# Kernel optimization log

Measured on AMD Instinct MI355X. Metric: run time of the kernel, lower is better.

## Reference

```python
import jax, jax.numpy as jnp
import numpy as np

B, N, F_IN, F_OUT = 8, 2048, 128, 128
ALPHA = 0.1  # leaky-relu negative slope
NEG = -9e15


def setup_inputs() -> dict:
    key = jax.random.key(0)
    k1, k2, k3, k4, k5, k6 = jax.random.split(key, 6)
    s = 1.0 / np.sqrt(F_OUT)
    return {
        "x1": jax.random.normal(k1, (B, N, F_IN), dtype=jnp.float32),
        "x2": jax.random.normal(k2, (B, N, F_IN), dtype=jnp.float32),
        "cross_weight": jax.random.uniform(k3, (F_IN, F_OUT), minval=-s, maxval=s, dtype=jnp.float32),
        "friend_weight": jax.random.uniform(k4, (F_IN, F_OUT), minval=-s, maxval=s, dtype=jnp.float32),
        "self_weight": jax.random.uniform(k5, (F_IN, F_OUT), minval=-s, maxval=s, dtype=jnp.float32),
        "att_weight": jax.random.uniform(k6, (2 * F_OUT, 1), minval=-1.0, maxval=1.0, dtype=jnp.float32),
    }


def _one_set(xq, x_others, cross_weight, friend_weight, self_weight, att_weight):
    # GAT-style additive attention for one set against cross-set + friend supports.
    fo = cross_weight.shape[1]
    a_q, a_k = att_weight[:fo], att_weight[fo:]  # split additive-attention vector
    cross = jnp.concatenate([xo @ cross_weight for xo in x_others], axis=1)  # [B, M, F]
    friend = xq @ friend_weight                                              # [B, Nq, F]
    h = jnp.concatenate([cross, friend], axis=1)                             # [B, Nk, F]
    s_q = (friend @ a_q)[..., 0]  # [B, Nq]
    s_k = (h @ a_k)[..., 0]       # [B, Nk]
    e = jax.nn.leaky_relu(s_q[:, :, None] + s_k[:, None, :], negative_slope=ALPHA)  # [B, Nq, Nk]
    nq, m = xq.shape[1], cross.shape[1]
    # mask: all cross-set keys allowed; friend keys masked on the diagonal (no self-edge)
    mask = jnp.concatenate([jnp.ones((nq, m), dtype=e.dtype),
                            1.0 - jnp.eye(nq, dtype=e.dtype)], axis=1)
    att = jax.nn.softmax(jnp.where(mask > 0, e, NEG), axis=-1)  # [B, Nq, Nk]
    out = jnp.einsum('bqk,bkf->bqf', att, h)                    # [B, Nq, F]
    return out + xq @ self_weight


def reference(x1, x2, cross_weight, friend_weight, self_weight, att_weight):
    out1 = _one_set(x1, [x2], cross_weight, friend_weight, self_weight, att_weight)
    out2 = _one_set(x2, [x1], cross_weight, friend_weight, self_weight, att_weight)
    return (out1, out2)
```

## Files before the change

### kernel.cpp

```cpp
#include <hip/hip_runtime.h>
#include <hip/hip_bf16.h>
#include <stdint.h>

typedef __attribute__((ext_vector_type(8))) short short8;
typedef __attribute__((ext_vector_type(16))) float f32x16;

#define NB 8
#define NN 2048
#define NF 128
#define NK 4096
#define L2E 1.4426950408889634f

#define OFF_HT   0u
#define OFF_WCT  16777216u
#define OFF_WFT  16809984u
#define OFF_WST  16842752u
#define OFF_U1   16875520u
#define OFF_U2   16876032u
#define OFF_U3   16876544u
#define OFF_SQ   16877056u
#define OFF_SK   17008128u

__device__ __forceinline__ short f2bf(float f){
  __bf16 h = (__bf16)f;
  return __builtin_bit_cast(short, h);
}
__device__ __forceinline__ short8 pack8(float4 a, float4 b){
  short8 r;
  r[0]=f2bf(a.x); r[1]=f2bf(a.y); r[2]=f2bf(a.z); r[3]=f2bf(a.w);
  r[4]=f2bf(b.x); r[5]=f2bf(b.y); r[6]=f2bf(b.z); r[7]=f2bf(b.w);
  return r;
}

typedef const __attribute__((address_space(1))) unsigned int* gas_t;
typedef __attribute__((address_space(3))) unsigned int* las_t;
__device__ __forceinline__ void gload_lds16(const void* g, void* l){
  __builtin_amdgcn_global_load_lds((gas_t)g, (las_t)l, 16, 0, 0);
}

__global__ __launch_bounds__(256) void k_prep(const float* __restrict__ Wc,
                                              const float* __restrict__ Wf,
                                              const float* __restrict__ Ws,
                                              const float* __restrict__ att,
                                              char* __restrict__ ws){
  int bidx = blockIdx.x, tid = threadIdx.x;
  if (bidx < 12){
    __shared__ float tile[32][129];
    int m = bidx >> 2, tno = bidx & 3;
    const float* W = (m == 0) ? Wc : ((m == 1) ? Wf : Ws);
    short* WT = (short*)(ws + ((m == 0) ? OFF_WCT : ((m == 1) ? OFF_WFT : OFF_WST)));
    int r0 = tno*32;
    #pragma unroll
    for (int i = 0; i < 16; i++){
      int e = tid + i*256;
      tile[e >> 7][e & 127] = W[(r0 + (e >> 7))*NF + (e & 127)];
    }
    __syncthreads();
    #pragma unroll
    for (int i = 0; i < 16; i++){
      int o = tid + i*256;
      int col = o >> 5, rr = o & 31;
      WT[col*NF + r0 + rr] = f2bf(tile[rr][col]);
    }
  } else {
    int wid = tid >> 6, lane = tid & 63;
    float aq0 = att[lane],      aq1 = att[64 + lane];
    float ak0 = att[NF + lane], ak1 = att[NF + 64 + lane];
    float* u1 = (float*)(ws + OFF_U1);
    float* u2 = (float*)(ws + OFF_U2);
    float* u3 = (float*)(ws + OFF_U3);
    for (int j = 0; j < 32; j++){
      int r = wid*32 + j;
      float wf0 = Wf[r*NF + lane], wf1 = Wf[r*NF + 64 + lane];
      float wc0 = Wc[r*NF + lane], wc1 = Wc[r*NF + 64 + lane];
      float s1 = wf0*aq0 + wf1*aq1;
      float s2 = wc0*ak0 + wc1*ak1;
      float s3 = wf0*ak0 + wf1*ak1;
      #pragma unroll
      for (int d = 1; d < 64; d <<= 1){
        s1 += __shfl_xor(s1, d); s2 += __shfl_xor(s2, d); s3 += __shfl_xor(s3, d);
      }
      if (lane == 0){ u1[r] = s1; u2[r] = s2; u3[r] = s3; }
    }
  }
}

__global__ __launch_bounds__(256) void k_build(const float* __restrict__ x1,
                                               const float* __restrict__ x2,
                                               char* __restrict__ ws){
  int bid = blockIdx.x;
  int xid  = bid >> 7;
  int b    = (bid >> 4) & 7;
  int tile = bid & 15;
  int tid = threadIdx.x, wid = tid >> 6, lane = tid & 63;
  int l31 = lane & 31, khalf = lane >> 5;
  int r0 = tile*128 + wid*32;
  int row = r0 + l31;

  const float* x = xid ? x2 : x1;
  const float* u1 = (const float*)(ws + OFF_U1);
  const float* u2 = (const float*)(ws + OFF_U2);
  const float* u3 = (const float*)(ws + OFF_U3);
  const float* xrow = x + (size_t)(b*NN + row)*NF;

  short8 aF[8];
  float p1=0.f, p2=0.f, p3=0.f;
  #pragma unroll
  for (int ks = 0; ks < 8; ks++){
    int k0 = ks*16 + khalf*8;
    float4 xa = *(const float4*)(xrow + k0);
    float4 xb = *(const float4*)(xrow + k0 + 4);
    float4 a1 = *(const float4*)(u1 + k0), b1 = *(const float4*)(u1 + k0 + 4);
    float4 a2 = *(const float4*)(u2 + k0), b2 = *(const float4*)(u2 + k0 + 4);
    float4 a3 = *(const float4*)(u3 + k0), b3 = *(const float4*)(u3 + k0 + 4);
    p1 += xa.x*a1.x + xa.y*a1.y + xa.z*a1.z + xa.w*a1.w
        + xb.x*b1.x + xb.y*b1.y + xb.z*b1.z + xb.w*b1.w;
    p2 += xa.x*a2.x + xa.y*a2.y + xa.z*a2.z + xa.w*a2.w
        + xb.x*b2.x + xb.y*b2.y + xb.z*b2.z + xb.w*b2.w;
    p3 += xa.x*a3.x + xa.y*a3.y + xa.z*a3.z + xa.w*a3.w
        + xb.x*b3.x + xb.y*b3.y + xb.z*b3.z + xb.w*b3.w;
    aF[ks] = pack8(xa, xb);
  }
  p1 += __shfl_xor(p1, 32);
  p2 += __shfl_xor(p2, 32);
  p3 += __shfl_xor(p3, 32);
  if (lane < 32){
    float* sq = (float*)(ws + OFF_SQ);
    float* sk = (float*)(ws + OFF_SK);
    sq[(xid*NB + b)*NN + row] = p1*L2E;
    sk[(xid*NB + b)*NK + NN + row] = p3*L2E;
    sk[((1 - xid)*NB + b)*NK + row] = p2*L2E;
  }

  short* hT = (short*)(ws + OFF_HT);
  #pragma unroll
  for (int g = 0; g < 2; g++){
    const short* W = g ? (const short*)(ws + OFF_WFT) : (const short*)(ws + OFF_WCT);
    int dset = g ? xid : (1 - xid);
    int kb2  = (g ? NN : 0) + r0;
    f32x16 acc[4] = {};
    #pragma unroll
    for (int ks = 0; ks < 8; ks++){
      #pragma unroll
      for (int cb = 0; cb < 4; cb++){
        short8 bF = *(const short8*)(W + (cb*32 + l31)*NF + ks*16 + khalf*8);
        acc[cb] = __builtin_amdgcn_mfma_f32_32x32x16_bf16(aF[ks], bF, acc[cb], 0, 0, 0);
      }
    }
    short* hbase = hT + (size_t)(dset*NB + b)*NF*NK;
    #pragma unroll
    for (int cb = 0; cb < 4; cb++){
      short* hc = hbase + (size_t)(cb*32 + l31)*NK;
      #pragma unroll
      for (int g4 = 0; g4 < 4; g4++){
        int kr = kb2 + g4*8 + khalf*4;
        uint2 v;
        v.x = (unsigned)(unsigned short)f2bf(acc[cb][4*g4+0]) |
              ((unsigned)(unsigned short)f2bf(acc[cb][4*g4+1]) << 16);
        v.y = (unsigned)(unsigned short)f2bf(acc[cb][4*g4+2]) |
              ((unsigned)(unsigned short)f2bf(acc[cb][4*g4+3]) << 16);
        *(uint2*)(hc + kr) = v;
      }
    }
  }
}

__global__ __launch_bounds__(512) void k_attn(const float* __restrict__ x1,
                                              const float* __restrict__ x2,
                                              const char* __restrict__ ws,
                                              float* __restrict__ out){
  __shared__ float skb[NK];
  __shared__ __align__(16) char stg[6*16384];
  __shared__ float wmax[8];

  int hw = blockIdx.x;
  int bid = (hw & 7)*32 + (hw >> 3);
  int set = bid >> 7, b = (bid >> 4) & 7, qt = bid & 15;
  int tid = threadIdx.x, wid = tid >> 6, lane = tid & 63;
  int grp = wid >> 2, rw = wid & 3;
  int l31 = lane & 31, khalf = lane >> 5;

  const short* hT  = (const short*)(ws + OFF_HT) + (size_t)(set*NB + b)*NF*NK;
  const float* skg = (const float*)(ws + OFF_SK) + (set*NB + b)*NK;
  const float* sqg = (const float*)(ws + OFF_SQ) + (set*NB + b)*NN;
  const short* WsT = (const short*)(ws + OFF_WST);

  auto stage = [&](int li, int bufi){
    char* dst = stg + (grp*3 + bufi)*16384;
    int ch = grp*32 + li;
    #pragma unroll
    for (int i = 0; i < 4; i++){
      int q = (rw*4 + i)*64 + lane;
      int col = q >> 3, k16 = q & 7;
      int srcc = k16 ^ (col & 7);
      gload_lds16((const void*)(hT + col*NK + ch*64 + srcc*8),
                  (void*)(dst + (rw*4 + i)*1024));
    }
  };

  stage(0, 0);
  stage(1, 1);
  float mx = -3.0e38f;
  #pragma unroll
  for (int i = 0; i < 2; i++){
    int idx = i*2048 + tid*4;
    float4 v = *(const float4*)(skg + idx);
    *(float4*)(skb + idx) = v;
    mx = fmaxf(mx, fmaxf(fmaxf(v.x, v.y), fmaxf(v.z, v.w)));
  }
  #pragma unroll
  for (int d = 1; d < 64; d <<= 1) mx = fmaxf(mx, __shfl_xor(mx, d));
  if (lane == 0) wmax[wid] = mx;
  asm volatile("s_waitcnt lgkmcnt(0)" ::: "memory");
  asm volatile("s_barrier" ::: "memory");

  float skmax = wmax[0];
  #pragma unroll
  for (int i = 1; i < 8; i++) skmax = fmaxf(skmax, wmax[i]);

  int q0w = qt*128 + rw*32;
  int row = q0w + l31;
  float sqv = sqg[row];
  float t0 = sqv + skmax;
  float moff = fmaxf(t0, 0.1f*t0);
  float sqm = sqv - moff;
  float c9  = -0.9f*moff;
  int kdiag = NN + row;
  int chd = (NN + q0w) >> 6;
  int ksd = (q0w & 63) >> 4;

  f32x16 acc[4] = {};
  float zacc = 0.f;

  int bs = 2, bc = 0;
  for (int it = 0; it < 32; ++it){
    if (it < 30){
      stage(it + 2, bs);
      asm volatile("s_waitcnt vmcnt(8)" ::: "memory");
    } else if (it == 30){
      asm volatile("s_waitcnt vmcnt(4)" ::: "memory");
    } else {
      asm volatile("s_waitcnt vmcnt(0)" ::: "memory");
    }
    asm volatile("s_barrier" ::: "memory");

    int ch = grp*32 + it;
    const char* buf = stg + (grp*3 + bc)*16384;
    #pragma unroll
    for (int ks = 0; ks < 4; ks++){
      const float* skp = skb + ch*64 + ks*16 + khalf*8;
      float wv[8];
      #pragma unroll
      for (int j = 0; j < 8; j++){
        float p = skp[j] + sqm;
        float qn = __builtin_fmaf(0.1f, p, c9);
        wv[j] = __builtin_amdgcn_exp2f(fmaxf(p, qn));
      }
      if (ch == chd && (ks & ~1) == ksd){
        int kg0 = ch*64 + ks*16 + khalf*8;
        #pragma unroll
        for (int j = 0; j < 8; j++) wv[j] = (kg0 + j == kdiag) ? 0.f : wv[j];
      }
      #pragma unroll
      for (int j = 0; j < 8; j++) zacc += wv[j];
      short8 aw;
      #pragma unroll
      for (int j = 0; j < 8; j++) aw[j] = f2bf(wv[j]);
      #pragma unroll
      for (int cb = 0; cb < 4; cb++){
        int col = cb*32 + l31;
        int slot = (ks*2 + khalf) ^ (col & 7);
        short8 bF = *(const short8*)(buf + col*128 + slot*16);
        acc[cb] = __builtin_amdgcn_mfma_f32_32x32x16_bf16(aw, bF, acc[cb], 0, 0, 0);
      }
    }
    asm volatile("s_barrier" ::: "memory");
    bs = (bs == 2) ? 0 : bs + 1;
    bc = (bc == 2) ? 0 : bc + 1;
  }

  float* xch = (float*)stg;
  float* zx  = skb;
  if (grp == 1){
    #pragma unroll
    for (int cb = 0; cb < 4; cb++)
      #pragma unroll
      for (int r = 0; r < 16; r++)
        xch[(cb*16 + r)*256 + rw*64 + lane] = acc[cb][r];
    zx[rw*64 + lane] = zacc;
  }
  __syncthreads();
  if (grp == 0){
    #pragma unroll
    for (int cb = 0; cb < 4; cb++)
      #pragma unroll
      for (int r = 0; r < 16; r++)
        acc[cb][r] += xch[(cb*16 + r)*256 + rw*64 + lane];
    zacc += zx[rw*64 + lane];
    zacc += __shfl_xor(zacc, 32);
    float rz = 1.0f / zacc;
    float rzv[16];
    #pragma unroll
    for (int r = 0; r < 16; r++){
      int rowc = (r & 3) + 8*(r >> 2) + 4*khalf;
      rzv[r] = __shfl(rz, rowc);
    }
    #pragma unroll
    for (int cb = 0; cb < 4; cb++)
      #pragma unroll
      for (int r = 0; r < 16; r++) acc[cb][r] *= rzv[r];

    const float* x = set ? x2 : x1;
    const float* xrow = x + (size_t)(b*NN + row)*NF;
    #pragma unroll
    for (int ks8 = 0; ks8 < 8; ks8++){
      int k0 = ks8*16 + khalf*8;
      float4 xa = *(const float4*)(xrow + k0);
      float4 xb = *(const float4*)(xrow + k0 + 4);
      short8 aF = pack8(xa, xb);
      #pragma unroll
      for (int cb = 0; cb < 4; cb++){
        short8 bF = *(const short8*)(WsT + (cb*32 + l31)*NF + k0);
        acc[cb] = __builtin_amdgcn_mfma_f32_32x32x16_bf16(aF, bF, acc[cb], 0, 0, 0);
      }
    }
    float* op = out + (size_t)(set*NB + b)*NN*NF;
    #pragma unroll
    for (int cb = 0; cb < 4; cb++){
      #pragma unroll
      for (int r = 0; r < 16; r++){
        int rowc = (r & 3) + 8*(r >> 2) + 4*khalf;
        op[(size_t)(q0w + rowc)*NF + cb*32 + l31] = acc[cb][r];
      }
    }
  }
}

extern "C" void kernel_launch(void* const* d_in, const int* in_sizes, int n_in,
                              void* d_out, int out_size, void* d_ws, size_t ws_size,
                              hipStream_t stream){
  const float* x1  = (const float*)d_in[0];
  const float* x2  = (const float*)d_in[1];
  const float* Wc  = (const float*)d_in[2];
  const float* Wf  = (const float*)d_in[3];
  const float* Ws  = (const float*)d_in[4];
  const float* att = (const float*)d_in[5];
  char* ws = (char*)d_ws;
  float* out = (float*)d_out;

  k_prep<<<dim3(13),  dim3(256), 0, stream>>>(Wc, Wf, Ws, att, ws);
  k_build<<<dim3(256), dim3(256), 0, stream>>>(x1, x2, ws);
  k_attn<<<dim3(256), dim3(512), 0, stream>>>(x1, x2, ws, out);
}
```

Baseline: 179.7 us.

## Split attention keys across four wave groups, each wave computing two row blocks

Restructures the attention kernel so each wave handles 64 query rows (two 32-row MFMA blocks) against a shared B fragment. The key range is split across four groups of two waves instead of two groups of four, and staging becomes double-buffered with larger 16KB-per-wave-pair chunks. The intent is to reuse each LDS-loaded h fragment for two MFMAs, halving LDS reads per FLOP. In exchange it doubles accumulator registers (128 floats per lane), raises LDS use to 128KB and adds a two-stage cross-group reduction with extra barriers. The launch bound of 2 blocks per CU may conflict with that LDS footprint or force register spills.

```diff
diff --git a/kernel.cpp b/kernel.cpp
--- a/kernel.cpp
+++ b/kernel.cpp
@@ -165,19 +165,19 @@
   }
 }
 
-__global__ __launch_bounds__(512) void k_attn(const float* __restrict__ x1,
+__global__ __launch_bounds__(512, 2) void k_attn(const float* __restrict__ x1,
                                               const float* __restrict__ x2,
                                               const char* __restrict__ ws,
                                               float* __restrict__ out){
   __shared__ float skb[NK];
-  __shared__ __align__(16) char stg[6*16384];
+  __shared__ __align__(16) char stg[8*16384];
   __shared__ float wmax[8];
 
   int hw = blockIdx.x;
   int bid = (hw & 7)*32 + (hw >> 3);
   int set = bid >> 7, b = (bid >> 4) & 7, qt = bid & 15;
   int tid = threadIdx.x, wid = tid >> 6, lane = tid & 63;
-  int grp = wid >> 2, rw = wid & 3;
+  int grp = wid >> 1, rw = wid & 1;
   int l31 = lane & 31, khalf = lane >> 5;
 
   const short* hT  = (const short*)(ws + OFF_HT) + (size_t)(set*NB + b)*NF*NK;
@@ -185,21 +185,20 @@
   const float* sqg = (const float*)(ws + OFF_SQ) + (set*NB + b)*NN;
   const short* WsT = (const short*)(ws + OFF_WST);
 
-  auto stage = [&](int li, int bufi){
-    char* dst = stg + (grp*3 + bufi)*16384;
-    int ch = grp*32 + li;
-    #pragma unroll
-    for (int i = 0; i < 4; i++){
-      int q = (rw*4 + i)*64 + lane;
-      int col = q >> 3, k16 = q & 7;
+  auto stage = [&](int it, int bufi){
+    char* dst = stg + (grp*2 + bufi)*16384;
+    int ch = grp*16 + it;
+    #pragma unroll
+    for (int i = 0; i < 8; i++){
+      int u = (rw*8 + i)*64 + lane;
+      int col = u >> 3, k16 = u & 7;
       int srcc = k16 ^ (col & 7);
       gload_lds16((const void*)(hT + col*NK + ch*64 + srcc*8),
-                  (void*)(dst + (rw*4 + i)*1024));
+                  (void*)(dst + (rw*8 + i)*1024));
     }
   };
 
   stage(0, 0);
-  stage(1, 1);
   float mx = -3.0e38f;
   #pragma unroll
   for (int i = 0; i < 2; i++){
@@ -218,120 +217,161 @@
   #pragma unroll
   for (int i = 1; i < 8; i++) skmax = fmaxf(skmax, wmax[i]);
 
-  int q0w = qt*128 + rw*32;
-  int row = q0w + l31;
-  float sqv = sqg[row];
-  float t0 = sqv + skmax;
-  float moff = fmaxf(t0, 0.1f*t0);
-  float sqm = sqv - moff;
-  float c9  = -0.9f*moff;
-  int kdiag = NN + row;
+  int q0w = qt*128 + rw*64;
+  float sqm[2], c9[2]; int kdiag[2];
+  #pragma unroll
+  for (int rb = 0; rb < 2; rb++){
+    int row = q0w + rb*32 + l31;
+    float sqv = sqg[row];
+    float t0 = sqv + skmax;
+    float moff = fmaxf(t0, 0.1f*t0);
+    sqm[rb] = sqv - moff;
+    c9[rb]  = -0.9f*moff;
+    kdiag[rb] = NN + row;
+  }
   int chd = (NN + q0w) >> 6;
-  int ksd = (q0w & 63) >> 4;
-
-  f32x16 acc[4] = {};
-  float zacc = 0.f;
-
-  int bs = 2, bc = 0;
-  for (int it = 0; it < 32; ++it){
-    if (it < 30){
-      stage(it + 2, bs);
+
+  f32x16 acc[2][4] = {};
+  float zacc[2] = {0.f, 0.f};
+
+  for (int it = 0; it < 16; ++it){
+    if (it < 15){
+      stage(it + 1, (it + 1) & 1);
       asm volatile("s_waitcnt vmcnt(8)" ::: "memory");
-    } else if (it == 30){
-      asm volatile("s_waitcnt vmcnt(4)" ::: "memory");
     } else {
       asm volatile("s_waitcnt vmcnt(0)" ::: "memory");
     }
     asm volatile("s_barrier" ::: "memory");
 
-    int ch = grp*32 + it;
-    const char* buf = stg + (grp*3 + bc)*16384;
+    int ch = grp*16 + it;
+    const char* buf = stg + (grp*2 + (it & 1))*16384;
     #pragma unroll
     for (int ks = 0; ks < 4; ks++){
       const float* skp = skb + ch*64 + ks*16 + khalf*8;
-      float wv[8];
-      #pragma unroll
-      for (int j = 0; j < 8; j++){
-        float p = skp[j] + sqm;
-        float qn = __builtin_fmaf(0.1f, p, c9);
-        wv[j] = __builtin_amdgcn_exp2f(fmaxf(p, qn));
-      }
-      if (ch == chd && (ks & ~1) == ksd){
-        int kg0 = ch*64 + ks*16 + khalf*8;
-        #pragma unroll
-        for (int j = 0; j < 8; j++) wv[j] = (kg0 + j == kdiag) ? 0.f : wv[j];
-      }
-      #pragma unroll
-      for (int j = 0; j < 8; j++) zacc += wv[j];
-      short8 aw;
-      #pragma unroll
-      for (int j = 0; j < 8; j++) aw[j] = f2bf(wv[j]);
+      float sv[8];
+      #pragma unroll
+      for (int j = 0; j < 8; j++) sv[j] = skp[j];
+      short8 aw[2];
+      #pragma unroll
+      for (int rb = 0; rb < 2; rb++){
+        float wv[8];
+        #pragma unroll
+        for (int j = 0; j < 8; j++){
+          float p = sv[j] + sqm[rb];
+          float qn = __builtin_fmaf(0.1f, p, c9[rb]);
+          wv[j] = __builtin_amdgcn_exp2f(fmaxf(p, qn));
+        }
+        if (ch == chd){
+          int kg0 = ch*64 + ks*16 + khalf*8;
+          #pragma unroll
+          for (int j = 0; j < 8; j++) wv[j] = (kg0 + j == kdiag[rb]) ? 0.f : wv[j];
+        }
+        #pragma unroll
+        for (int j = 0; j < 8; j++) zacc[rb] += wv[j];
+        #pragma unroll
+        for (int j = 0; j < 8; j++) aw[rb][j] = f2bf(wv[j]);
+      }
       #pragma unroll
       for (int cb = 0; cb < 4; cb++){
         int col = cb*32 + l31;
         int slot = (ks*2 + khalf) ^ (col & 7);
         short8 bF = *(const short8*)(buf + col*128 + slot*16);
-        acc[cb] = __builtin_amdgcn_mfma_f32_32x32x16_bf16(aw, bF, acc[cb], 0, 0, 0);
+        acc[0][cb] = __builtin_amdgcn_mfma_f32_32x32x16_bf16(aw[0], bF, acc[0][cb], 0, 0, 0);
+        acc[1][cb] = __builtin_amdgcn_mfma_f32_32x32x16_bf16(aw[1], bF, acc[1][cb], 0, 0, 0);
       }
     }
     asm volatile("s_barrier" ::: "memory");
-    bs = (bs == 2) ? 0 : bs + 1;
-    bc = (bc == 2) ? 0 : bc + 1;
-  }
-
-  float* xch = (float*)stg;
-  float* zx  = skb;
-  if (grp == 1){
-    #pragma unroll
-    for (int cb = 0; cb < 4; cb++)
-      #pragma unroll
-      for (int r = 0; r < 16; r++)
-        xch[(cb*16 + r)*256 + rw*64 + lane] = acc[cb][r];
-    zx[rw*64 + lane] = zacc;
+  }
+
+  float* cbuf1 = (float*)stg;
+  float* cbuf2 = (float*)(stg + 65536);
+  float* zarr  = skb;
+  if (grp == 1 || grp == 3){
+    float* dst = (grp == 1) ? cbuf1 : cbuf2;
+    #pragma unroll
+    for (int rb = 0; rb < 2; rb++){
+      #pragma unroll
+      for (int cb = 0; cb < 4; cb++)
+        #pragma unroll
+        for (int r = 0; r < 16; r++)
+          dst[(((rw*2 + rb)*4 + cb)*16 + r)*64 + lane] = acc[rb][cb][r];
+      zarr[(wid*2 + rb)*64 + lane] = zacc[rb];
+    }
+  }
+  __syncthreads();
+  if (grp == 0 || grp == 2){
+    const float* src = (grp == 0) ? cbuf1 : cbuf2;
+    int swid = (grp == 0) ? (2 + rw) : (6 + rw);
+    #pragma unroll
+    for (int rb = 0; rb < 2; rb++){
+      #pragma unroll
+      for (int cb = 0; cb < 4; cb++)
+        #pragma unroll
+        for (int r = 0; r < 16; r++)
+          acc[rb][cb][r] += src[(((rw*2 + rb)*4 + cb)*16 + r)*64 + lane];
+      zacc[rb] += zarr[(swid*2 + rb)*64 + lane];
+    }
+  }
+  __syncthreads();
+  if (grp == 2){
+    #pragma unroll
+    for (int rb = 0; rb < 2; rb++){
+      #pragma unroll
+      for (int cb = 0; cb < 4; cb++)
+        #pragma unroll
+        for (int r = 0; r < 16; r++)
+          cbuf1[(((rw*2 + rb)*4 + cb)*16 + r)*64 + lane] = acc[rb][cb][r];
+      zarr[((4 + rw)*2 + rb)*64 + lane] = zacc[rb];
+    }
   }
   __syncthreads();
   if (grp == 0){
     #pragma unroll
-    for (int cb = 0; cb < 4; cb++)
-      #pragma unroll
-      for (int r = 0; r < 16; r++)
-        acc[cb][r] += xch[(cb*16 + r)*256 + rw*64 + lane];
-    zacc += zx[rw*64 + lane];
-    zacc += __shfl_xor(zacc, 32);
-    float rz = 1.0f / zacc;
-    float rzv[16];
-    #pragma unroll
-    for (int r = 0; r < 16; r++){
-      int rowc = (r & 3) + 8*(r >> 2) + 4*khalf;
-      rzv[r] = __shfl(rz, rowc);
-    }
-    #pragma unroll
-    for (int cb = 0; cb < 4; cb++)
-      #pragma unroll
-      for (int r = 0; r < 16; r++) acc[cb][r] *= rzv[r];
-
+    for (int rb = 0; rb < 2; rb++){
+      #pragma unroll
+      for (int cb = 0; cb < 4; cb++)
+        #pragma unroll
+        for (int r = 0; r < 16; r++)
+          acc[rb][cb][r] += cbuf1[(((rw*2 + rb)*4 + cb)*16 + r)*64 + lane];
+      zacc[rb] += zarr[((4 + rw)*2 + rb)*64 + lane];
+    }
     const float* x = set ? x2 : x1;
-    const float* xrow = x + (size_t)(b*NN + row)*NF;
-    #pragma unroll
-    for (int ks8 = 0; ks8 < 8; ks8++){
-      int k0 = ks8*16 + khalf*8;
-      float4 xa = *(const float4*)(xrow + k0);
-      float4 xb = *(const float4*)(xrow + k0 + 4);
-      short8 aF = pack8(xa, xb);
-      #pragma unroll
-      for (int cb = 0; cb < 4; cb++){
-        short8 bF = *(const short8*)(WsT + (cb*32 + l31)*NF + k0);
-        acc[cb] = __builtin_amdgcn_mfma_f32_32x32x16_bf16(aF, bF, acc[cb], 0, 0, 0);
-      }
-    }
     float* op = out + (size_t)(set*NB + b)*NN*NF;
     #pragma unroll
-    for (int cb = 0; cb < 4; cb++){
+    for (int rb = 0; rb < 2; rb++){
+      float zr = zacc[rb] + __shfl_xor(zacc[rb], 32);
+      float rz = 1.0f / zr;
+      float rzv[16];
       #pragma unroll
       for (int r = 0; r < 16; r++){
         int rowc = (r & 3) + 8*(r >> 2) + 4*khalf;
-        op[(size_t)(q0w + rowc)*NF + cb*32 + l31] = acc[cb][r];
-      }
+        rzv[r] = __shfl(rz, rowc);
+      }
+      #pragma unroll
+      for (int cb = 0; cb < 4; cb++)
+        #pragma unroll
+        for (int r = 0; r < 16; r++) acc[rb][cb][r] *= rzv[r];
+
+      const float* xrow = x + (size_t)(b*NN + q0w + rb*32 + l31)*NF;
+      #pragma unroll
+      for (int ks8 = 0; ks8 < 8; ks8++){
+        int k0 = ks8*16 + khalf*8;
+        float4 xa = *(const float4*)(xrow + k0);
+        float4 xb = *(const float4*)(xrow + k0 + 4);
+        short8 aF = pack8(xa, xb);
+        #pragma unroll
+        for (int cb = 0; cb < 4; cb++){
+          short8 bF = *(const short8*)(WsT + (cb*32 + l31)*NF + k0);
+          acc[rb][cb] = __builtin_amdgcn_mfma_f32_32x32x16_bf16(aF, bF, acc[rb][cb], 0, 0, 0);
+        }
+      }
+      #pragma unroll
+      for (int cb = 0; cb < 4; cb++)
+        #pragma unroll
+        for (int r = 0; r < 16; r++){
+          int rowc = (r & 3) + 8*(r >> 2) + 4*khalf;
+          op[(size_t)(q0w + rb*32 + rowc)*NF + cb*32 + l31] = acc[rb][cb][r];
+        }
     }
   }
 }
```

Result: faster. 171.9 us (-4.4%).
